# Performance work log

Hardware: AMD Instinct MI355X
Metric: run time of the kernel (lower is better)

## Reference

```python
import jax, jax.numpy as jnp
import numpy as np

DIM = 1024
SEQ_LEN = 2048
NUM_HEAD = 16
HEAD_DIM = 64
B = 4


def setup_inputs() -> dict:
    key = jax.random.key(0)
    ks = jax.random.split(key, 9)
    hd = NUM_HEAD * HEAD_DIM
    s_in = 1.0 / np.sqrt(DIM)
    s_o = 1.0 / np.sqrt(hd)
    return {
        "x": jax.random.normal(ks[0], (B, SEQ_LEN, DIM), dtype=jnp.float32),
        "q_w": jax.random.uniform(ks[1], (hd, DIM), jnp.float32, -s_in, s_in),
        "q_b": jax.random.uniform(ks[2], (hd,), jnp.float32, -s_in, s_in),
        "k_w": jax.random.uniform(ks[3], (hd, DIM), jnp.float32, -s_in, s_in),
        "k_b": jax.random.uniform(ks[4], (hd,), jnp.float32, -s_in, s_in),
        "v_w": jax.random.uniform(ks[5], (hd, DIM), jnp.float32, -s_in, s_in),
        "v_b": jax.random.uniform(ks[6], (hd,), jnp.float32, -s_in, s_in),
        "o_w": jax.random.uniform(ks[7], (DIM, hd), jnp.float32, -s_o, s_o),
        "o_b": jax.random.uniform(ks[8], (DIM,), jnp.float32, -s_o, s_o),
    }


def reference(x, q_w, q_b, k_w, k_b, v_w, v_b, o_w, o_b):
    Bn, T, C = x.shape
    # QKV projections (torch Linear: x @ W^T + b)
    q = (x @ q_w.T + q_b).reshape(Bn, T, NUM_HEAD, HEAD_DIM).transpose(0, 2, 1, 3)
    k = (x @ k_w.T + k_b).reshape(Bn, T, NUM_HEAD, HEAD_DIM).transpose(0, 2, 1, 3)
    v = (x @ v_w.T + v_b).reshape(Bn, T, NUM_HEAD, HEAD_DIM).transpose(0, 2, 1, 3)
    scale = HEAD_DIM ** -0.5
    attn = jnp.einsum("bhqd,bhkd->bhqk", q, k) * scale  # (B,H,T,T)
    causal = jnp.tril(jnp.ones((T, T), dtype=bool))
    attn = jnp.where(causal[None, None, :, :], attn, -jnp.inf)
    p = jax.nn.softmax(attn, axis=-1)  # stable softmax (max-subtracted)
    out = jnp.einsum("bhqk,bhkd->bhqd", p, v)
    out = out.transpose(0, 2, 1, 3).reshape(Bn, T, NUM_HEAD * HEAD_DIM)
    return out @ o_w.T + o_b
```

## Files before the change

### kernel.cpp

```cpp
#include <hip/hip_runtime.h>
#include <stdint.h>

typedef short short8 __attribute__((ext_vector_type(8)));
typedef float f32x4 __attribute__((ext_vector_type(4)));
typedef float f32x16 __attribute__((ext_vector_type(16)));
typedef unsigned int uint2v __attribute__((ext_vector_type(2)));
typedef unsigned int uint4v __attribute__((ext_vector_type(4)));

__device__ __forceinline__ unsigned short f2bf(float f) {
    unsigned int u = __float_as_uint(f);
    u += 0x7fffu + ((u >> 16) & 1u);
    return (unsigned short)(u >> 16);
}

__device__ __forceinline__ void gld_lds16(const unsigned short* g, unsigned short* l) {
    __builtin_amdgcn_global_load_lds((const __attribute__((address_space(1))) unsigned int*)g,
                                     (__attribute__((address_space(3))) unsigned int*)l,
                                     16, 0, 0);
}

#define QSCL 0.18033688011112042f

__global__ __launch_bounds__(256) void cvt_all(const float* __restrict__ x,
                                               const float* __restrict__ qw, const float* __restrict__ kw,
                                               const float* __restrict__ vw, const float* __restrict__ ow,
                                               const float* __restrict__ qb, const float* __restrict__ kb,
                                               const float* __restrict__ vb,
                                               unsigned short* __restrict__ Xb,
                                               unsigned short* __restrict__ Wqkv,
                                               unsigned short* __restrict__ Owb,
                                               float* __restrict__ bqkv) {
    int i = blockIdx.x * 256 + threadIdx.x;
    const float* src; uint2* dst; int j;
    if (i < 2097152)      { src = x;  dst = (uint2*)Xb;                j = i; }
    else if (i < 2359296) { src = qw; dst = (uint2*)Wqkv;              j = i - 2097152; }
    else if (i < 2621440) { src = kw; dst = (uint2*)(Wqkv + 1048576);  j = i - 2359296; }
    else if (i < 2883584) { src = vw; dst = (uint2*)(Wqkv + 2097152);  j = i - 2621440; }
    else if (i < 3145728) { src = ow; dst = (uint2*)Owb;               j = i - 2883584; }
    else {
        int t = i - 3145728;
        const float4* bs = (t < 256) ? (const float4*)qb : (t < 512) ? (const float4*)kb : (const float4*)vb;
        ((float4*)bqkv)[t] = bs[t & 255];
        return;
    }
    float4 v = ((const float4*)src)[j];
    unsigned int lo = (unsigned int)f2bf(v.x) | ((unsigned int)f2bf(v.y) << 16);
    unsigned int hi = (unsigned int)f2bf(v.z) | ((unsigned int)f2bf(v.w) << 16);
    dst[j] = make_uint2(lo, hi);
}

template<int MODE>
__global__ __launch_bounds__(256) void gemm_bt(const unsigned short* __restrict__ A,
                                               const unsigned short* __restrict__ Bm,
                                               const float* __restrict__ bias,
                                               void* __restrict__ C0,
                                               unsigned short* __restrict__ VtOut,
                                               int M, int N, int K)
{
    __shared__ __align__(16) unsigned short As[128 * 64];
    __shared__ __align__(16) unsigned short Bs[128 * 64];
    const int tid  = threadIdx.x;
    const int bm   = blockIdx.x, bn = blockIdx.y;
    const int lane = tid & 63, w = tid >> 6;
    const int wm   = w >> 1, wn = w & 1;
    const int quad = lane >> 4, l15 = lane & 15;

    f32x4 acc[4][4];
#pragma unroll
    for (int mt = 0; mt < 4; mt++)
#pragma unroll
        for (int nt = 0; nt < 4; nt++)
            acc[mt][nt] = (f32x4){0.f, 0.f, 0.f, 0.f};

    const int kTiles = K >> 6;
    for (int kt = 0; kt < kTiles; ++kt) {
        __syncthreads();
#pragma unroll
        for (int i = 0; i < 4; i++) {
            int G  = i * 256 + tid;
            int m  = G >> 3, g = G & 7;
            int gs = g ^ (m & 7);
            int Gb = i * 256 + (w << 6);
            gld_lds16(A  + (size_t)(bm * 128 + m) * K + kt * 64 + gs * 8, &As[Gb * 8]);
            gld_lds16(Bm + (size_t)(bn * 128 + m) * K + kt * 64 + gs * 8, &Bs[Gb * 8]);
        }
        __syncthreads();
#pragma unroll
        for (int ks = 0; ks < 2; ++ks) {
            short8 af[4], bfr[4];
#pragma unroll
            for (int mt = 0; mt < 4; mt++) {
                int m = wm * 64 + mt * 16 + l15;
                af[mt] = *(const short8*)&As[m * 64 + (((ks * 4 + quad) ^ (l15 & 7)) << 3)];
            }
#pragma unroll
            for (int nt = 0; nt < 4; nt++) {
                int n = wn * 64 + nt * 16 + l15;
                bfr[nt] = *(const short8*)&Bs[n * 64 + (((ks * 4 + quad) ^ (l15 & 7)) << 3)];
            }
#pragma unroll
            for (int mt = 0; mt < 4; mt++)
#pragma unroll
                for (int nt = 0; nt < 4; nt++)
                    acc[mt][nt] = __builtin_amdgcn_mfma_f32_16x16x32_bf16(af[mt], bfr[nt], acc[mt][nt], 0, 0, 0);
        }
    }
    const int row0 = bm * 128 + wm * 64, col0 = bn * 128 + wn * 64;
#pragma unroll
    for (int nt = 0; nt < 4; nt++) {
        int col = col0 + nt * 16 + l15;
        float bv = bias[col];
#pragma unroll
        for (int mt = 0; mt < 4; mt++) {
            if (MODE == 1 && col >= 2048) {
                int row = row0 + mt * 16 + quad * 4;
                int b = row >> 11, t = row & 2047;
                ushort4 pk;
                pk.x = f2bf(acc[mt][nt][0] + bv);
                pk.y = f2bf(acc[mt][nt][1] + bv);
                pk.z = f2bf(acc[mt][nt][2] + bv);
                pk.w = f2bf(acc[mt][nt][3] + bv);
                *(ushort4*)(VtOut + (size_t)(b * 1024 + (col - 2048)) * 2048 + t) = pk;
            } else {
#pragma unroll
                for (int r = 0; r < 4; r++) {
                    int row = row0 + mt * 16 + quad * 4 + r;
                    float v = acc[mt][nt][r] + bv;
                    if (MODE == 1) {
                        if (col < 1024) v *= QSCL;
                        ((unsigned short*)C0)[(size_t)row * 2048 + col] = f2bf(v);
                    } else {
                        ((float*)C0)[(size_t)row * N + col] = v;
                    }
                }
            }
        }
    }
}

#define NEG_RAW (-1e30f)
__global__ __launch_bounds__(256, 4) void attn_mfma(const unsigned short* __restrict__ QK,
                                                    const unsigned short* __restrict__ Vt,
                                                    unsigned short* __restrict__ O)
{
    __shared__ __align__(16) unsigned short Kb[2][64 * 64];
    __shared__ __align__(16) unsigned short Vb[2][64 * 64];
    const int tid  = threadIdx.x;
    const int lane = tid & 63, w = tid >> 6;
    const int hi   = lane >> 5, l31 = lane & 31;
    const int s7   = lane & 7;
    const int bh   = blockIdx.x;
    const int b    = bh >> 4, h = bh & 15;
    const int qt   = (int)gridDim.y - 1 - (int)blockIdx.y;
    const int qbase = qt * 128 + w * 32;

    const unsigned short* Qp = QK + (size_t)(b * 2048) * 2048 + h * 64;
    const unsigned short* Kp = Qp + 1024;
    const unsigned short* Vp = Vt + (size_t)(bh * 64) * 2048;

    short8 qf[4];
    {
        const unsigned short* qrow = Qp + (size_t)(qbase + l31) * 2048 + hi * 8;
#pragma unroll
        for (int dk = 0; dk < 4; dk++)
            qf[dk] = *(const short8*)(qrow + dk * 16);
    }

    f32x16 oacc[2];
#pragma unroll
    for (int i = 0; i < 2; i++)
#pragma unroll
        for (int r = 0; r < 16; r++) oacc[i][r] = 0.f;
    float lsum = 0.f;

    const int ktend   = 2 * qt + 1;
    const int ktmax_w = (qbase + 31) >> 6;

#pragma unroll
    for (int i = 0; i < 2; i++) {
        int G = i * 256 + tid;
        int r = G >> 3, g = G & 7, gs = g ^ (r & 7);
        int Gb = i * 256 + (w << 6);
        gld_lds16(Kp + (size_t)r * 2048 + gs * 8, &Kb[0][Gb * 8]);
        gld_lds16(Vp + (size_t)r * 2048 + gs * 8, &Vb[0][Gb * 8]);
    }
    __syncthreads();

    for (int kt = 0; kt <= ktend; ++kt) {
        const int cur = kt & 1;
        if (kt < ktend) {
            const unsigned short* Kn = Kp + (size_t)((kt + 1) * 64) * 2048;
            const unsigned short* Vn = Vp + (kt + 1) * 64;
#pragma unroll
            for (int i = 0; i < 2; i++) {
                int G = i * 256 + tid;
                int r = G >> 3, g = G & 7, gs = g ^ (r & 7);
                int Gb = i * 256 + (w << 6);
                gld_lds16(Kn + (size_t)r * 2048 + gs * 8, &Kb[cur ^ 1][Gb * 8]);
                gld_lds16(Vn + (size_t)r * 2048 + gs * 8, &Vb[cur ^ 1][Gb * 8]);
            }
        }
        if (kt <= ktmax_w) {
            __builtin_amdgcn_s_setprio(1);
            const unsigned short* Kc = Kb[cur];
            const unsigned short* Vc = Vb[cur];
            const int kbase = kt * 64;
#pragma unroll
            for (int sub = 0; sub < 2; sub++) {
                const int kb0 = kbase + sub * 32;
                if (kb0 > qbase + 31) continue;
                f32x16 sacc;
#pragma unroll
                for (int r = 0; r < 16; r++) sacc[r] = 0.f;
                const unsigned short* kr = &Kc[(sub * 32 + l31) * 64];
#pragma unroll
                for (int dk = 0; dk < 4; dk++) {
                    short8 kf = *(const short8*)(kr + (((dk * 2 + hi) ^ s7) << 3));
                    sacc = __builtin_amdgcn_mfma_f32_32x32x16_bf16(kf, qf[dk], sacc, 0, 0, 0);
                }
                if (kb0 + 31 > qbase) {
                    const int qg = qbase + l31;
                    const int kb = kb0 + 4 * hi;
#pragma unroll
                    for (int r = 0; r < 16; r++) {
                        int key = kb + (r & 3) + 8 * (r >> 2);
                        if (key > qg) sacc[r] = NEG_RAW;
                    }
                }
#pragma unroll
                for (int r = 0; r < 16; r++) sacc[r] = __builtin_exp2f(sacc[r]);
                {
                    float s0 = (sacc[0] + sacc[1]) + (sacc[2] + sacc[3]);
                    float s1 = (sacc[4] + sacc[5]) + (sacc[6] + sacc[7]);
                    float s2 = (sacc[8] + sacc[9]) + (sacc[10] + sacc[11]);
                    float s3 = (sacc[12] + sacc[13]) + (sacc[14] + sacc[15]);
                    lsum += (s0 + s1) + (s2 + s3);
                }
                unsigned int pk[8];
#pragma unroll
                for (int t2 = 0; t2 < 8; t2++)
                    pk[t2] = __builtin_amdgcn_perm(__float_as_uint(sacc[2 * t2 + 1]),
                                                   __float_as_uint(sacc[2 * t2]), 0x07060302u);
                uint2v r0 = __builtin_amdgcn_permlane32_swap(pk[0], pk[2], false, false);
                uint2v r1 = __builtin_amdgcn_permlane32_swap(pk[1], pk[3], false, false);
                uint2v r2 = __builtin_amdgcn_permlane32_swap(pk[4], pk[6], false, false);
                uint2v r3 = __builtin_amdgcn_permlane32_swap(pk[5], pk[7], false, false);
                short8 pf[2];
                { uint4v u; u.x = r0.x; u.y = r1.x; u.z = r0.y; u.w = r1.y; pf[0] = __builtin_bit_cast(short8, u); }
                { uint4v u; u.x = r2.x; u.y = r3.x; u.z = r2.y; u.w = r3.y; pf[1] = __builtin_bit_cast(short8, u); }
#pragma unroll
                for (int kv = 0; kv < 2; kv++) {
#pragma unroll
                    for (int dsub = 0; dsub < 2; dsub++) {
                        const int d = dsub * 32 + l31;
                        short8 vf = *(const short8*)&Vc[d * 64 + (((sub * 4 + kv * 2 + hi) ^ s7) << 3)];
                        oacc[dsub] = __builtin_amdgcn_mfma_f32_32x32x16_bf16(vf, pf[kv], oacc[dsub], 0, 0, 0);
                    }
                }
            }
            __builtin_amdgcn_s_setprio(0);
        }
        __syncthreads();
    }

    uint2v lt = __builtin_amdgcn_permlane32_swap(__float_as_uint(lsum), __float_as_uint(lsum), false, false);
    const float inv = 1.f / (__uint_as_float(lt.x) + __uint_as_float(lt.y));
    unsigned short* op = O + (size_t)(b * 2048 + qbase + l31) * 1024 + h * 64;
#pragma unroll
    for (int dsub = 0; dsub < 2; dsub++) {
#pragma unroll
        for (int q4 = 0; q4 < 4; q4++) {
            ushort4 pkv;
            pkv.x = f2bf(oacc[dsub][q4 * 4 + 0] * inv);
            pkv.y = f2bf(oacc[dsub][q4 * 4 + 1] * inv);
            pkv.z = f2bf(oacc[dsub][q4 * 4 + 2] * inv);
            pkv.w = f2bf(oacc[dsub][q4 * 4 + 3] * inv);
            *(ushort4*)(op + dsub * 32 + q4 * 8 + hi * 4) = pkv;
        }
    }
}

extern "C" void kernel_launch(void* const* d_in, const int* in_sizes, int n_in,
                              void* d_out, int out_size, void* d_ws, size_t ws_size,
                              hipStream_t stream)
{
    const float* x   = (const float*)d_in[0];
    const float* q_w = (const float*)d_in[1];
    const float* q_b = (const float*)d_in[2];
    const float* k_w = (const float*)d_in[3];
    const float* k_b = (const float*)d_in[4];
    const float* v_w = (const float*)d_in[5];
    const float* v_b = (const float*)d_in[6];
    const float* o_w = (const float*)d_in[7];
    const float* o_b = (const float*)d_in[8];
    float* out = (float*)d_out;

    unsigned short* Xb   = (unsigned short*)d_ws;
    unsigned short* Wqkv = Xb + 8388608;
    unsigned short* Owb  = Wqkv + 3145728;
    float*          bqkv = (float*)(Owb + 1048576);
    unsigned short* QK   = (unsigned short*)(bqkv + 3072);
    unsigned short* Vtg  = QK + 16777216;
    unsigned short* Abf  = Vtg + 8388608;

    cvt_all<<<12291, 256, 0, stream>>>(x, q_w, k_w, v_w, o_w, q_b, k_b, v_b,
                                       Xb, Wqkv, Owb, bqkv);
    gemm_bt<1><<<dim3(64, 24), 256, 0, stream>>>(Xb, Wqkv, bqkv, QK, Vtg, 8192, 3072, 1024);
    attn_mfma<<<dim3(64, 16), 256, 0, stream>>>(QK, Vtg, Abf);
    gemm_bt<0><<<dim3(64, 8), 256, 0, stream>>>(Abf, Owb, o_b, out, nullptr, 8192, 1024, 1024);
}
```

Measured before the change: 255.6 us.

## Replace 128x128 GEMM with 256x256 double-buffered ping-pong MFMA pipeline

Both projection GEMMs move to a new kernel with 256x256 output tiles and 512 threads (8 waves, 128x64 per wave). LDS is double-buffered, and global-to-LDS staging of the next K tiles is interleaved in quarters between MFMA groups. Scheduling is controlled explicitly with sched barriers, s_setprio and manual vmcnt waits. The larger tiles cut global/LDS traffic per flop and the interleaving hides load latency. In exchange, LDS use is about 128KB per block and the grids shrink a lot, to 384 and 128 blocks, which may leave CUs idle on the output projection.

Measured after the change: 275.1 us. +7.6%, slower.

```diff
diff --git a/kernel.cpp b/kernel.cpp
--- a/kernel.cpp
+++ b/kernel.cpp
@@ -49,69 +49,138 @@
     dst[j] = make_uint2(lo, hi);
 }
 
+
+#define BAR() do { __builtin_amdgcn_sched_barrier(0); __builtin_amdgcn_s_barrier(); \
+                   __builtin_amdgcn_sched_barrier(0); } while (0)
+
+#define RD_A(BI, MH) \
+    _Pragma("unroll") for (int mtl = 0; mtl < 4; ++mtl) { \
+        int m = wm * 128 + (MH) * 64 + mtl * 16 + l15; \
+        af[mtl][0] = *(const short8*)&As[BI][m * 64 + ((quad ^ (m & 7)) << 3)]; \
+        af[mtl][1] = *(const short8*)&As[BI][m * 64 + (((4 + quad) ^ (m & 7)) << 3)]; \
+    }
+
+#define RD_B(BI, NH) \
+    _Pragma("unroll") for (int ntl = 0; ntl < 2; ++ntl) { \
+        int n = wn * 64 + ((NH) * 2 + ntl) * 16 + l15; \
+        bfv[(NH) * 2 + ntl][0] = *(const short8*)&Bs[BI][n * 64 + ((quad ^ (n & 7)) << 3)]; \
+        bfv[(NH) * 2 + ntl][1] = *(const short8*)&Bs[BI][n * 64 + (((4 + quad) ^ (n & 7)) << 3)]; \
+    }
+
+#define MFMA_Q(MH, NH) \
+    __builtin_amdgcn_s_setprio(1); \
+    _Pragma("unroll") for (int mtl = 0; mtl < 4; ++mtl) \
+    _Pragma("unroll") for (int ntl = 0; ntl < 2; ++ntl) { \
+        const int nt_ = (NH) * 2 + ntl, mt_ = (MH) * 4 + mtl; \
+        acc[mt_][nt_] = __builtin_amdgcn_mfma_f32_16x16x32_bf16(af[mtl][0], bfv[nt_][0], acc[mt_][nt_], 0, 0, 0); \
+        acc[mt_][nt_] = __builtin_amdgcn_mfma_f32_16x16x32_bf16(af[mtl][1], bfv[nt_][1], acc[mt_][nt_], 0, 0, 0); \
+    } \
+    __builtin_amdgcn_s_setprio(0);
+
+#define STAGE(DST, BI, H, SRC, KT) \
+    _Pragma("unroll") for (int i_ = 0; i_ < 2; ++i_) { \
+        int G_ = i_ * 512 + tid; \
+        int r_ = G_ >> 3, g_ = G_ & 7, gs_ = g_ ^ (r_ & 7); \
+        gld_lds16((SRC) + (size_t)((H) * 128 + r_) * K + (KT) * 64 + gs_ * 8, \
+                  &DST[BI][(H) * 8192 + (i_ * 512 + w * 64) * 8]); \
+    }
+
 template<int MODE>
-__global__ __launch_bounds__(256) void gemm_bt(const unsigned short* __restrict__ A,
-                                               const unsigned short* __restrict__ Bm,
-                                               const float* __restrict__ bias,
-                                               void* __restrict__ C0,
-                                               unsigned short* __restrict__ VtOut,
-                                               int M, int N, int K)
+__global__ __launch_bounds__(512, 2) void gemm256(const unsigned short* __restrict__ A,
+                                                  const unsigned short* __restrict__ Bm,
+                                                  const float* __restrict__ bias,
+                                                  void* __restrict__ C0,
+                                                  unsigned short* __restrict__ VtOut,
+                                                  int M, int N, int K)
 {
-    __shared__ __align__(16) unsigned short As[128 * 64];
-    __shared__ __align__(16) unsigned short Bs[128 * 64];
+    __shared__ __align__(16) unsigned short As[2][256 * 64];
+    __shared__ __align__(16) unsigned short Bs[2][256 * 64];
     const int tid  = threadIdx.x;
     const int bm   = blockIdx.x, bn = blockIdx.y;
     const int lane = tid & 63, w = tid >> 6;
-    const int wm   = w >> 1, wn = w & 1;
+    const int wm   = w >> 2, wn = w & 3;
     const int quad = lane >> 4, l15 = lane & 15;
 
-    f32x4 acc[4][4];
-#pragma unroll
-    for (int mt = 0; mt < 4; mt++)
+    const unsigned short* Ag = A  + (size_t)(bm * 256) * K;
+    const unsigned short* Bg = Bm + (size_t)(bn * 256) * K;
+
+    f32x4 acc[8][4];
+#pragma unroll
+    for (int mt = 0; mt < 8; mt++)
 #pragma unroll
         for (int nt = 0; nt < 4; nt++)
             acc[mt][nt] = (f32x4){0.f, 0.f, 0.f, 0.f};
 
-    const int kTiles = K >> 6;
-    for (int kt = 0; kt < kTiles; ++kt) {
-        __syncthreads();
-#pragma unroll
-        for (int i = 0; i < 4; i++) {
-            int G  = i * 256 + tid;
-            int m  = G >> 3, g = G & 7;
-            int gs = g ^ (m & 7);
-            int Gb = i * 256 + (w << 6);
-            gld_lds16(A  + (size_t)(bm * 128 + m) * K + kt * 64 + gs * 8, &As[Gb * 8]);
-            gld_lds16(Bm + (size_t)(bn * 128 + m) * K + kt * 64 + gs * 8, &Bs[Gb * 8]);
-        }
-        __syncthreads();
-#pragma unroll
-        for (int ks = 0; ks < 2; ++ks) {
-            short8 af[4], bfr[4];
-#pragma unroll
-            for (int mt = 0; mt < 4; mt++) {
-                int m = wm * 64 + mt * 16 + l15;
-                af[mt] = *(const short8*)&As[m * 64 + (((ks * 4 + quad) ^ (l15 & 7)) << 3)];
-            }
-#pragma unroll
-            for (int nt = 0; nt < 4; nt++) {
-                int n = wn * 64 + nt * 16 + l15;
-                bfr[nt] = *(const short8*)&Bs[n * 64 + (((ks * 4 + quad) ^ (l15 & 7)) << 3)];
-            }
-#pragma unroll
-            for (int mt = 0; mt < 4; mt++)
-#pragma unroll
-                for (int nt = 0; nt < 4; nt++)
-                    acc[mt][nt] = __builtin_amdgcn_mfma_f32_16x16x32_bf16(af[mt], bfr[nt], acc[mt][nt], 0, 0, 0);
-        }
-    }
-    const int row0 = bm * 128 + wm * 64, col0 = bn * 128 + wn * 64;
+    short8 af[4][2];
+    short8 bfv[4][2];
+
+    const int NI = K >> 7;
+
+    STAGE(As, 0, 0, Ag, 0); STAGE(As, 0, 1, Ag, 0);
+    STAGE(Bs, 0, 0, Bg, 0); STAGE(Bs, 0, 1, Bg, 0);
+    STAGE(Bs, 1, 0, Bg, 1); STAGE(Bs, 1, 1, Bg, 1);
+    asm volatile("s_waitcnt vmcnt(4)" ::: "memory");
+    BAR();
+
+    for (int j = 0; j < NI; ++j) {
+        const int t1 = 2 * j + 1, t2 = 2 * j + 2, t3 = 2 * j + 3;
+        const bool more = (j < NI - 1);
+        RD_A(0, 0); RD_B(0, 0);
+        __builtin_amdgcn_sched_barrier(0);
+        STAGE(As, 1, 0, Ag, t1);
+        BAR();
+        MFMA_Q(0, 0);
+        BAR();
+        RD_B(0, 1);
+        __builtin_amdgcn_sched_barrier(0);
+        STAGE(As, 1, 1, Ag, t1);
+        BAR();
+        MFMA_Q(0, 1);
+        BAR();
+        RD_A(0, 1);
+        __builtin_amdgcn_sched_barrier(0);
+        if (more) { STAGE(Bs, 0, 0, Bg, t2); }
+        BAR();
+        MFMA_Q(1, 0);
+        BAR();
+        if (more) { STAGE(Bs, 0, 1, Bg, t2); }
+        BAR();
+        MFMA_Q(1, 1);
+        if (more) { asm volatile("s_waitcnt vmcnt(4)" ::: "memory"); }
+        else      { asm volatile("s_waitcnt vmcnt(0)" ::: "memory"); }
+        BAR();
+        RD_A(1, 0); RD_B(1, 0);
+        __builtin_amdgcn_sched_barrier(0);
+        if (more) { STAGE(As, 0, 0, Ag, t2); }
+        BAR();
+        MFMA_Q(0, 0);
+        BAR();
+        RD_B(1, 1);
+        __builtin_amdgcn_sched_barrier(0);
+        if (more) { STAGE(As, 0, 1, Ag, t2); }
+        BAR();
+        MFMA_Q(0, 1);
+        BAR();
+        RD_A(1, 1);
+        __builtin_amdgcn_sched_barrier(0);
+        if (more) { STAGE(Bs, 1, 0, Bg, t3); }
+        BAR();
+        MFMA_Q(1, 0);
+        BAR();
+        if (more) { STAGE(Bs, 1, 1, Bg, t3); }
+        BAR();
+        MFMA_Q(1, 1);
+        if (more) { asm volatile("s_waitcnt vmcnt(4)" ::: "memory"); }
+        BAR();
+    }
+
+    const int row0 = bm * 256 + wm * 128, col0 = bn * 256 + wn * 64;
 #pragma unroll
     for (int nt = 0; nt < 4; nt++) {
         int col = col0 + nt * 16 + l15;
         float bv = bias[col];
 #pragma unroll
-        for (int mt = 0; mt < 4; mt++) {
+        for (int mt = 0; mt < 8; mt++) {
             if (MODE == 1 && col >= 2048) {
                 int row = row0 + mt * 16 + quad * 4;
                 int b = row >> 11, t = row & 2047;
@@ -305,7 +374,7 @@
 
     cvt_all<<<12291, 256, 0, stream>>>(x, q_w, k_w, v_w, o_w, q_b, k_b, v_b,
                                        Xb, Wqkv, Owb, bqkv);
-    gemm_bt<1><<<dim3(64, 24), 256, 0, stream>>>(Xb, Wqkv, bqkv, QK, Vtg, 8192, 3072, 1024);
+    gemm256<1><<<dim3(32, 12), 512, 0, stream>>>(Xb, Wqkv, bqkv, QK, Vtg, 8192, 3072, 1024);
     attn_mfma<<<dim3(64, 16), 256, 0, stream>>>(QK, Vtg, Abf);
-    gemm_bt<0><<<dim3(64, 8), 256, 0, stream>>>(Abf, Owb, o_b, out, nullptr, 8192, 1024, 1024);
-}
+    gemm256<0><<<dim3(32, 4), 512, 0, stream>>>(Abf, Owb, o_b, out, nullptr, 8192, 1024, 1024);
+}
```

## Triple-buffer K/V tiles in attention with prefetch depth two and manual waitcnt

Applied to the files above, without the earlier changes.

Moves the attention kernel's K/V staging from double to triple buffering in LDS. Tiles are now prefetched two iterations ahead, with an explicit s_waitcnt on vmcnt and one raw barrier per iteration replacing the trailing __syncthreads. The aim is to hide global-to-LDS load latency better and remove one barrier per loop. In exchange LDS use grows from 32KB to 48KB per block, which may cut occupancy under the 4-blocks-per-CU launch bound, and correctness now depends on the hand-written vmcnt count.

After: 255.2 us. No clear change (-0.2%).

```diff
diff --git a/kernel.cpp b/kernel.cpp
--- a/kernel.cpp
+++ b/kernel.cpp
@@ -143,8 +143,8 @@
                                                     const unsigned short* __restrict__ Vt,
                                                     unsigned short* __restrict__ O)
 {
-    __shared__ __align__(16) unsigned short Kb[2][64 * 64];
-    __shared__ __align__(16) unsigned short Vb[2][64 * 64];
+    __shared__ __align__(16) unsigned short Kb[3][64 * 64];
+    __shared__ __align__(16) unsigned short Vb[3][64 * 64];
     const int tid  = threadIdx.x;
     const int lane = tid & 63, w = tid >> 6;
     const int hi   = lane >> 5, l31 = lane & 31;
@@ -176,29 +176,30 @@
     const int ktend   = 2 * qt + 1;
     const int ktmax_w = (qbase + 31) >> 6;
 
-#pragma unroll
-    for (int i = 0; i < 2; i++) {
-        int G = i * 256 + tid;
-        int r = G >> 3, g = G & 7, gs = g ^ (r & 7);
-        int Gb = i * 256 + (w << 6);
-        gld_lds16(Kp + (size_t)r * 2048 + gs * 8, &Kb[0][Gb * 8]);
-        gld_lds16(Vp + (size_t)r * 2048 + gs * 8, &Vb[0][Gb * 8]);
-    }
-    __syncthreads();
-
+    auto stage = [&](int t, int bi) {
+#pragma unroll
+        for (int i = 0; i < 2; i++) {
+            int G = i * 256 + tid;
+            int r = G >> 3, g = G & 7, gs = g ^ (r & 7);
+            int Gb = i * 256 + (w << 6);
+            gld_lds16(Kp + (size_t)(t * 64 + r) * 2048 + gs * 8, &Kb[bi][Gb * 8]);
+            gld_lds16(Vp + (size_t)r * 2048 + t * 64 + gs * 8, &Vb[bi][Gb * 8]);
+        }
+    };
+
+    stage(0, 0);
+    stage(1, 1);
+
+    int cur = 0;
     for (int kt = 0; kt <= ktend; ++kt) {
-        const int cur = kt & 1;
-        if (kt < ktend) {
-            const unsigned short* Kn = Kp + (size_t)((kt + 1) * 64) * 2048;
-            const unsigned short* Vn = Vp + (kt + 1) * 64;
-#pragma unroll
-            for (int i = 0; i < 2; i++) {
-                int G = i * 256 + tid;
-                int r = G >> 3, g = G & 7, gs = g ^ (r & 7);
-                int Gb = i * 256 + (w << 6);
-                gld_lds16(Kn + (size_t)r * 2048 + gs * 8, &Kb[cur ^ 1][Gb * 8]);
-                gld_lds16(Vn + (size_t)r * 2048 + gs * 8, &Vb[cur ^ 1][Gb * 8]);
-            }
+        if (kt < ktend) asm volatile("s_waitcnt vmcnt(4)" ::: "memory");
+        else            asm volatile("s_waitcnt vmcnt(0)" ::: "memory");
+        __builtin_amdgcn_sched_barrier(0);
+        __builtin_amdgcn_s_barrier();
+        __builtin_amdgcn_sched_barrier(0);
+        if (kt + 2 <= ktend) {
+            int bi = cur + 2; if (bi >= 3) bi -= 3;
+            stage(kt + 2, bi);
         }
         if (kt <= ktmax_w) {
             __builtin_amdgcn_s_setprio(1);
@@ -260,7 +261,7 @@
             }
             __builtin_amdgcn_s_setprio(0);
         }
-        __syncthreads();
+        cur = (cur == 2) ? 0 : cur + 1;
     }
 
     uint2v lt = __builtin_amdgcn_permlane32_swap(__float_as_uint(lsum), __float_as_uint(lsum), false, false);
```
